# Performance work log

Measured on AMD Instinct MI355X. Metric: run time of the kernel, lower is better.

The kernel has to match this reference:

```python
import jax, jax.numpy as jnp
import numpy as np

HEADS = 8
D_K = 64
LN_EPS = 1e-6


def setup_inputs() -> dict:
    key = jax.random.key(0)
    ks = jax.random.split(key, 12)
    B, S, D = 4, 2048, 512
    inp = {
        "key": jax.random.normal(ks[0], (B, S, D), jnp.float32),
        "value": jax.random.normal(ks[1], (B, S, D), jnp.float32),
        "query": jax.random.normal(ks[2], (B, S, D), jnp.float32),
        "mask": jax.random.randint(ks[3], (B, S, S), 0, 2).astype(bool),
        # projection weights (torch Linear: y = x @ W.T + b)
        "Wk": jax.random.normal(ks[4], (D, D), jnp.float32) * (1.0 / np.sqrt(D)),
        "bk": jnp.zeros((D,), jnp.float32),
        "Wv": jax.random.normal(ks[5], (D, D), jnp.float32) * (1.0 / np.sqrt(D)),
        "bv": jnp.zeros((D,), jnp.float32),
        "Wq": jax.random.normal(ks[6], (D, D), jnp.float32) * (1.0 / np.sqrt(D)),
        "bq": jnp.zeros((D,), jnp.float32),
        # LayerNorm gain/bias
        "a2": jnp.ones((D,), jnp.float32),
        "b2": jnp.zeros((D,), jnp.float32),
    }
    return inp


def _attention(key, value, query, mask, Wk, bk, Wv, bv, Wq, bq, a2, b2):
    B, Sq, D = query.shape
    Sk = key.shape[1]
    H, dk = HEADS, D_K

    def split_heads(x, W, b):
        y = x @ W.T + b                                   # [B, S, D]
        return y.reshape(x.shape[0], x.shape[1], H, dk).transpose(0, 2, 1, 3)  # [B,H,S,dk]

    k_up = split_heads(key, Wk, bk)
    v_up = split_heads(value, Wv, bv)
    q_up = split_heads(query, Wq, bq)

    # scaled dot-product scores, full [B,H,Sq,Sk] matrix (as in the original bmm)
    scores = jnp.einsum("bhqd,bhkd->bhqk", q_up, k_up) / jnp.sqrt(jnp.asarray(dk, scores_dtype(q_up)))
    scores = jnp.where(mask[:, None, :, :], -jnp.inf, scores)
    attn = jax.nn.softmax(scores, axis=-1)                # dropout p=0 -> identity

    out = jnp.einsum("bhqk,bhkd->bhqd", attn, v_up)       # [B,H,Sq,dk]
    out = out.transpose(0, 2, 1, 3).reshape(B, Sq, D)
    res = out + query                                     # residual (res_dropout p=0)

    # OpenNMT LayerNorm: (x - mu) / (std + eps) * a2 + b2, unbiased std
    mu = res.mean(axis=-1, keepdims=True)
    var = jnp.sum((res - mu) ** 2, axis=-1, keepdims=True) / (D - 1)
    res = a2 * (res - mu) / (jnp.sqrt(var) + LN_EPS) + b2

    attn_flat = attn.reshape(B * H, Sq, Sk)               # matches torch [B*H, Sq, Sk]
    return res, attn_flat


def scores_dtype(x):
    return x.dtype


def reference(key, value, query, mask, Wk, bk, Wv, bv, Wq, bq, a2, b2):
    return _attention(key, value, query, mask, Wk, bk, Wv, bv, Wq, bq, a2, b2)
```

## Files before the change

### kernel.cpp

```cpp
#include <hip/hip_runtime.h>
#include <stdint.h>

typedef float f32x4 __attribute__((ext_vector_type(4)));
typedef short bf16x8 __attribute__((ext_vector_type(8)));

constexpr int NB = 4;
constexpr int NS = 2048;
constexpr int ND = 512;
constexpr int NH = 8;
constexpr int NDK = 64;
constexpr int NT = NS / 64;
constexpr float QSCALE = 0.125f * 1.44269504088896340736f;

static __device__ __forceinline__ unsigned short f2bf(float f) {
    union { float f; uint32_t u; } v; v.f = f;
    uint32_t r = (v.u + 0x7FFFu + ((v.u >> 16) & 1u)) >> 16;
    return (unsigned short)r;
}
static __device__ __forceinline__ uint32_t pkbf(float a, float b) {
    union { float f; uint32_t u; } x, y; x.f = a; y.f = b;
    return ((x.u + 0x8000u) >> 16) | (((y.u + 0x8000u) >> 16) << 16);
}
static __device__ __forceinline__ float exp2_fast(float x) {
#if __has_builtin(__builtin_amdgcn_exp2f)
    return __builtin_amdgcn_exp2f(x);
#else
    return exp2f(x);
#endif
}

static __device__ __forceinline__ void gload_lds16(const void* g, void* l) {
    __builtin_amdgcn_global_load_lds((const __attribute__((address_space(1))) void*)g,
                                     (__attribute__((address_space(3))) void*)l, 16, 0, 0);
}

__global__ __launch_bounds__(256) void cvt3_kernel(const float4* __restrict__ a,
                                                   const float4* __restrict__ b,
                                                   const float4* __restrict__ c,
                                                   ushort4* __restrict__ oa,
                                                   ushort4* __restrict__ ob,
                                                   ushort4* __restrict__ oc, int n4) {
    int which = blockIdx.y;
    const float4* in = which == 0 ? a : which == 1 ? b : c;
    ushort4* out = which == 0 ? oa : which == 1 ? ob : oc;
    int i = blockIdx.x * blockDim.x + threadIdx.x;
    if (i >= n4) return;
    float4 v = in[i];
    ushort4 o;
    o.x = f2bf(v.x); o.y = f2bf(v.y); o.z = f2bf(v.z); o.w = f2bf(v.w);
    out[i] = o;
}

__global__ __launch_bounds__(256) void bitmask_kernel(const int* __restrict__ mask,
                                                      unsigned long long* __restrict__ bm,
                                                      int nwords) {
    int lane = threadIdx.x & 63;
    int wave = threadIdx.x >> 6;
    int wgid = blockIdx.x * 4 + wave;
    int nw = gridDim.x * 4;
    for (int c = wgid; c < nwords; c += nw) {
        int v = mask[(size_t)c * 64 + lane];
        unsigned long long bits = __ballot(v != 0);
        if (lane == 0) bm[c] = bits;
    }
}

__global__ __launch_bounds__(256) void proj_kernel(const unsigned short* __restrict__ xq,
                                                   const unsigned short* __restrict__ xk,
                                                   const unsigned short* __restrict__ xv,
                                                   const unsigned short* __restrict__ wq,
                                                   const unsigned short* __restrict__ wk,
                                                   const unsigned short* __restrict__ wv,
                                                   const float* __restrict__ bq,
                                                   const float* __restrict__ bk,
                                                   const float* __restrict__ bv,
                                                   unsigned short* __restrict__ Qw,
                                                   unsigned short* __restrict__ Kw,
                                                   unsigned short* __restrict__ VTw) {
    int z = blockIdx.z;
    const unsigned short* X = z == 0 ? xq : z == 1 ? xk : xv;
    const unsigned short* W = z == 0 ? wq : z == 1 ? wk : wv;
    const float* bias = z == 0 ? bq : z == 1 ? bk : bv;
    unsigned short* out = z == 0 ? Qw : z == 1 ? Kw : VTw;
    float scale = z == 0 ? QSCALE : 1.0f;
    int vtrans = (z == 2);

    int lane = threadIdx.x & 63;
    int wave = threadIdx.x >> 6;
    int lrow = lane & 15, lgrp = lane >> 4;
    int m0 = blockIdx.x * 64 + wave * 16;
    int n0 = blockIdx.y * 64;

    f32x4 acc[4] = {{0.f,0.f,0.f,0.f},{0.f,0.f,0.f,0.f},{0.f,0.f,0.f,0.f},{0.f,0.f,0.f,0.f}};
    const unsigned short* xrow = X + (size_t)(m0 + lrow) * ND;
    for (int k = 0; k < ND; k += 32) {
        bf16x8 a = *(const bf16x8*)(xrow + k + lgrp * 8);
#pragma unroll
        for (int n = 0; n < 4; n++) {
            bf16x8 b = *(const bf16x8*)(W + (size_t)(n0 + n * 16 + lrow) * ND + k + lgrp * 8);
            acc[n] = __builtin_amdgcn_mfma_f32_16x16x32_bf16(a, b, acc[n], 0, 0, 0);
        }
    }
#pragma unroll
    for (int n = 0; n < 4; n++) {
        int col = n0 + n * 16 + lrow;
        int h = col >> 6, d = col & 63;
        float bv_ = bias[col];
#pragma unroll
        for (int j = 0; j < 4; j++) {
            int m = m0 + lgrp * 4 + j;
            int bidx = m >> 11, s = m & (NS - 1);
            float y = (acc[n][j] + bv_) * scale;
            size_t off = vtrans ? ((size_t)(bidx * NH + h) * NDK + d) * NS + s
                                : ((size_t)(bidx * NH + h) * NS + s) * NDK + d;
            out[off] = f2bf(y);
        }
    }
}

__global__ __launch_bounds__(512) void attn_kernel(const unsigned short* __restrict__ Q,
                                                   const unsigned short* __restrict__ K,
                                                   const unsigned short* __restrict__ VT,
                                                   const unsigned long long* __restrict__ bm,
                                                   float* __restrict__ attn_out,
                                                   float* __restrict__ Ob) {
    __shared__ __align__(16) unsigned short kb[2][64 * 64];
    __shared__ __align__(16) unsigned short vb[2][64 * 64];
    __shared__ __align__(16) unsigned short pl[8][16][72];

    int lane = threadIdx.x & 63;
    int wave = threadIdx.x >> 6;
    int lrow = lane & 15, lgrp = lane >> 4;

    int id = blockIdx.x;
    int xcd = id & 7;
    int loc = id >> 3;
    int bh = xcd * 4 + (loc >> 4);
    int qb = loc & 15;
    int b = bh >> 3, h = bh & 7;
    int qw = qb * 128 + wave * 16;

    const unsigned short* qrow = Q + ((size_t)bh * NS + qw + lrow) * NDK + lgrp * 8;
    bf16x8 aq0 = *(const bf16x8*)(qrow);
    bf16x8 aq1 = *(const bf16x8*)(qrow + 32);

    const unsigned short* kbase = K + (size_t)bh * NS * NDK;
    const unsigned short* vbase = VT + (size_t)bh * NDK * NS;
    const unsigned long long* bmrow = bm + ((size_t)b * NS + qw + lrow) * (NS / 64);

    int rl = lane >> 3, cc = lane & 7;
    int cs = (cc ^ rl) * 8;

    gload_lds16(kbase + (size_t)(8 * wave + rl) * NDK + cs, &kb[0][wave * 512]);
    unsigned long long wc = bmrow[0], wn = 0;
    asm volatile("s_waitcnt vmcnt(1)" ::: "memory");
    __builtin_amdgcn_s_barrier();

    float lacc = 0.f;
    for (int t = 0; t < NT; t++) {
        int buf = t & 1;
        if (t + 1 < NT) {
            gload_lds16(kbase + (size_t)((t + 1) * 64 + 8 * wave + rl) * NDK + cs,
                        &kb[buf ^ 1][wave * 512]);
            wn = bmrow[t + 1];
        }
        f32x4 sc[4] = {{0.f,0.f,0.f,0.f},{0.f,0.f,0.f,0.f},{0.f,0.f,0.f,0.f},{0.f,0.f,0.f,0.f}};
        __builtin_amdgcn_s_setprio(1);
#pragma unroll
        for (int n = 0; n < 4; n++) {
            int R = n * 16 + lrow;
            bf16x8 b0 = *(const bf16x8*)&kb[buf][R * 64 + ((lgrp ^ (lrow & 7)) * 8)];
            bf16x8 b1 = *(const bf16x8*)&kb[buf][R * 64 + (((4 + lgrp) ^ (lrow & 7)) * 8)];
            sc[n] = __builtin_amdgcn_mfma_f32_16x16x32_bf16(b0, aq0, sc[n], 0, 0, 0);
            sc[n] = __builtin_amdgcn_mfma_f32_16x16x32_bf16(b1, aq1, sc[n], 0, 0, 0);
        }
        __builtin_amdgcn_s_setprio(0);
        uint32_t wlo = (uint32_t)wc, whi = (uint32_t)(wc >> 32);
#pragma unroll
        for (int n = 0; n < 4; n++)
#pragma unroll
            for (int j = 0; j < 4; j++) {
                uint32_t bit = ((n < 2 ? wlo : whi) >> ((n & 1) * 16 + lgrp * 4 + j)) & 1u;
                float e = exp2_fast(sc[n][j]);
                lacc += bit ? 0.f : e;
            }
        wc = wn;
        if (t + 1 < NT) {
            asm volatile("s_waitcnt vmcnt(1)" ::: "memory");
            __builtin_amdgcn_s_barrier();
        }
    }
    lacc += __shfl_xor(lacc, 16);
    lacc += __shfl_xor(lacc, 32);
    float li = -__log2f(lacc);

    gload_lds16(kbase + (size_t)(8 * wave + rl) * NDK + cs, &kb[0][wave * 512]);
    gload_lds16(vbase + (size_t)(8 * wave + rl) * NS + cs, &vb[0][wave * 512]);
    wc = bmrow[0];
    asm volatile("s_waitcnt vmcnt(1)" ::: "memory");
    __builtin_amdgcn_s_barrier();

    f32x4 accO[4] = {{0.f,0.f,0.f,0.f},{0.f,0.f,0.f,0.f},{0.f,0.f,0.f,0.f},{0.f,0.f,0.f,0.f}};
    float* arow = attn_out + (size_t)bh * NS * NS + (size_t)(qw + lrow) * NS;

    for (int t = 0; t < NT; t++) {
        int buf = t & 1;
        int kt = t * 64;
        if (t + 1 < NT) {
            gload_lds16(kbase + (size_t)((t + 1) * 64 + 8 * wave + rl) * NDK + cs,
                        &kb[buf ^ 1][wave * 512]);
            gload_lds16(vbase + (size_t)(8 * wave + rl) * NS + (t + 1) * 64 + cs,
                        &vb[buf ^ 1][wave * 512]);
            wn = bmrow[t + 1];
        }
        f32x4 sc[4] = {{0.f,0.f,0.f,0.f},{0.f,0.f,0.f,0.f},{0.f,0.f,0.f,0.f},{0.f,0.f,0.f,0.f}};
        __builtin_amdgcn_s_setprio(1);
#pragma unroll
        for (int n = 0; n < 4; n++) {
            int R = n * 16 + lrow;
            bf16x8 b0 = *(const bf16x8*)&kb[buf][R * 64 + ((lgrp ^ (lrow & 7)) * 8)];
            bf16x8 b1 = *(const bf16x8*)&kb[buf][R * 64 + (((4 + lgrp) ^ (lrow & 7)) * 8)];
            sc[n] = __builtin_amdgcn_mfma_f32_16x16x32_bf16(b0, aq0, sc[n], 0, 0, 0);
            sc[n] = __builtin_amdgcn_mfma_f32_16x16x32_bf16(b1, aq1, sc[n], 0, 0, 0);
        }
        __builtin_amdgcn_s_setprio(0);
        uint32_t wlo = (uint32_t)wc, whi = (uint32_t)(wc >> 32);
#pragma unroll
        for (int n = 0; n < 4; n++) {
            float p0, p1, p2, p3;
            uint32_t wsel = (n < 2) ? wlo : whi;
            int base = (n & 1) * 16 + lgrp * 4;
            p0 = ((wsel >> (base + 0)) & 1u) ? 0.f : exp2_fast(sc[n][0] + li);
            p1 = ((wsel >> (base + 1)) & 1u) ? 0.f : exp2_fast(sc[n][1] + li);
            p2 = ((wsel >> (base + 2)) & 1u) ? 0.f : exp2_fast(sc[n][2] + li);
            p3 = ((wsel >> (base + 3)) & 1u) ? 0.f : exp2_fast(sc[n][3] + li);
            f32x4 pv4 = {p0, p1, p2, p3};
            __builtin_nontemporal_store(pv4, (f32x4*)(arow + kt + n * 16 + lgrp * 4));
            uint2 pk = {pkbf(p0, p1), pkbf(p2, p3)};
            *(uint2*)&pl[wave][lrow][n * 16 + lgrp * 4] = pk;
        }
        __builtin_amdgcn_s_setprio(1);
#pragma unroll
        for (int step = 0; step < 2; step++) {
            bf16x8 ap = *(const bf16x8*)&pl[wave][lrow][step * 32 + lgrp * 8];
#pragma unroll
            for (int n = 0; n < 4; n++) {
                int R = n * 16 + lrow;
                bf16x8 bv = *(const bf16x8*)&vb[buf][R * 64 + (((4 * step + lgrp) ^ (lrow & 7)) * 8)];
                accO[n] = __builtin_amdgcn_mfma_f32_16x16x32_bf16(ap, bv, accO[n], 0, 0, 0);
            }
        }
        __builtin_amdgcn_s_setprio(0);
        wc = wn;
        if (t + 1 < NT) {
            asm volatile("s_waitcnt vmcnt(5)" ::: "memory");
            __builtin_amdgcn_s_barrier();
        }
    }

#pragma unroll
    for (int n = 0; n < 4; n++)
#pragma unroll
        for (int j = 0; j < 4; j++) {
            int qi = qw + lgrp * 4 + j;
            Ob[((size_t)b * NS + qi) * ND + h * NDK + n * 16 + lrow] = accO[n][j];
        }
}

__global__ __launch_bounds__(256) void ln_kernel(const float* __restrict__ Ob,
                                                 const float* __restrict__ query,
                                                 const float* __restrict__ a2,
                                                 const float* __restrict__ b2,
                                                 float* __restrict__ out) {
    int row = blockIdx.x * 4 + (threadIdx.x >> 6);
    int lane = threadIdx.x & 63;
    const float4* orow = (const float4*)(Ob + (size_t)row * ND);
    const float4* qrow = (const float4*)(query + (size_t)row * ND);
    float4 v[2];
    float sum = 0.f;
#pragma unroll
    for (int t = 0; t < 2; t++) {
        float4 o = orow[lane + t * 64];
        float4 q = qrow[lane + t * 64];
        v[t].x = o.x + q.x; v[t].y = o.y + q.y; v[t].z = o.z + q.z; v[t].w = o.w + q.w;
        sum += v[t].x + v[t].y + v[t].z + v[t].w;
    }
#pragma unroll
    for (int s = 1; s < 64; s <<= 1) sum += __shfl_xor(sum, s);
    float mu = sum * (1.f / ND);
    float sq = 0.f;
#pragma unroll
    for (int t = 0; t < 2; t++) {
        float dx = v[t].x - mu, dy = v[t].y - mu, dz = v[t].z - mu, dw = v[t].w - mu;
        sq += dx * dx + dy * dy + dz * dz + dw * dw;
    }
#pragma unroll
    for (int s = 1; s < 64; s <<= 1) sq += __shfl_xor(sq, s);
    float var = sq * (1.f / (ND - 1));
    float inv = 1.f / (sqrtf(var) + 1e-6f);
    float4* orow_out = (float4*)(out + (size_t)row * ND);
#pragma unroll
    for (int t = 0; t < 2; t++) {
        float4 g = ((const float4*)a2)[lane + t * 64];
        float4 bb = ((const float4*)b2)[lane + t * 64];
        float4 r;
        r.x = g.x * (v[t].x - mu) * inv + bb.x;
        r.y = g.y * (v[t].y - mu) * inv + bb.y;
        r.z = g.z * (v[t].z - mu) * inv + bb.z;
        r.w = g.w * (v[t].w - mu) * inv + bb.w;
        orow_out[lane + t * 64] = r;
    }
}

extern "C" void kernel_launch(void* const* d_in, const int* in_sizes, int n_in,
                              void* d_out, int out_size, void* d_ws, size_t ws_size,
                              hipStream_t stream) {
    const float* key   = (const float*)d_in[0];
    const float* value = (const float*)d_in[1];
    const float* query = (const float*)d_in[2];
    const int*   mask  = (const int*)d_in[3];
    const float* Wk = (const float*)d_in[4];
    const float* bk = (const float*)d_in[5];
    const float* Wv = (const float*)d_in[6];
    const float* bv = (const float*)d_in[7];
    const float* Wq = (const float*)d_in[8];
    const float* bq = (const float*)d_in[9];
    const float* a2 = (const float*)d_in[10];
    const float* b2 = (const float*)d_in[11];

    const size_t nX = (size_t)NB * NS * ND;
    const size_t nW = (size_t)ND * ND;
    const int    nBMw = NB * NS * NS / 64;

    unsigned short* xq  = (unsigned short*)d_ws;
    unsigned short* xk  = xq + nX;
    unsigned short* xv  = xk + nX;
    unsigned short* wqb = xv + nX;
    unsigned short* wkb = wqb + nW;
    unsigned short* wvb = wkb + nW;
    unsigned short* Qw  = wvb + nW;
    unsigned short* Kw  = Qw + nX;
    unsigned short* VTw = Kw + nX;
    float* Ow = (float*)(VTw + nX);
    unsigned long long* bmw = (unsigned long long*)(Ow + nX);

    bitmask_kernel<<<2048, 256, 0, stream>>>(mask, bmw, nBMw);

    cvt3_kernel<<<dim3((int)(nX / 4 / 256), 3), 256, 0, stream>>>(
        (const float4*)query, (const float4*)key, (const float4*)value,
        (ushort4*)xq, (ushort4*)xk, (ushort4*)xv, (int)(nX / 4));
    cvt3_kernel<<<dim3((int)(nW / 4 / 256), 3), 256, 0, stream>>>(
        (const float4*)Wq, (const float4*)Wk, (const float4*)Wv,
        (ushort4*)wqb, (ushort4*)wkb, (ushort4*)wvb, (int)(nW / 4));

    proj_kernel<<<dim3(128, 8, 3), 256, 0, stream>>>(xq, xk, xv, wqb, wkb, wvb,
                                                     bq, bk, bv, Qw, Kw, VTw);

    float* attn_out = (float*)d_out + nX;
    attn_kernel<<<512, 512, 0, stream>>>(Qw, Kw, VTw, bmw, attn_out, Ow);

    ln_kernel<<<2048, 256, 0, stream>>>(Ow, query, a2, b2, (float*)d_out);
}
```

Measured before the change: 362.7 us.

## Split softmax row-sum pass into separate key-split kernel with atomic accumulation

The first pass of the attention kernel, which computes each query row's exp-sum over all keys, moves into its own kernel. That kernel splits the key range four ways across a second grid dimension and adds partial sums into a zeroed buffer with atomics. The attention kernel then reads the finished row sums and runs only the second pass. The goal is more parallelism for the serial row-sum pass, since the main kernel launches only 512 blocks. In exchange there is an extra memset and launch, K is read directly from global memory without LDS staging, and atomics make the float summation order nondeterministic.

```diff
diff --git a/kernel.cpp b/kernel.cpp
--- a/kernel.cpp
+++ b/kernel.cpp
@@ -118,10 +118,61 @@
     }
 }
 
+__global__ __launch_bounds__(512) void lsum_kernel(const unsigned short* __restrict__ Q,
+                                                   const unsigned short* __restrict__ K,
+                                                   const unsigned long long* __restrict__ bm,
+                                                   float* __restrict__ lsum) {
+    int lane = threadIdx.x & 63;
+    int wave = threadIdx.x >> 6;
+    int lrow = lane & 15, lgrp = lane >> 4;
+
+    int id = blockIdx.x;
+    int xcd = id & 7;
+    int loc = id >> 3;
+    int bh = xcd * 4 + (loc >> 4);
+    int qb = loc & 15;
+    int b = bh >> 3;
+    int qw = qb * 128 + wave * 16;
+    int kt0 = blockIdx.y * (NS / 4), kt1 = kt0 + NS / 4;
+
+    const unsigned short* qrow = Q + ((size_t)bh * NS + qw + lrow) * NDK + lgrp * 8;
+    bf16x8 aq0 = *(const bf16x8*)(qrow);
+    bf16x8 aq1 = *(const bf16x8*)(qrow + 32);
+    const unsigned short* kbase = K + (size_t)bh * NS * NDK;
+    const unsigned long long* bmrow = bm + ((size_t)b * NS + qw + lrow) * (NS / 64);
+
+    float lacc = 0.f;
+    for (int kt = kt0; kt < kt1; kt += 64) {
+        unsigned long long w = bmrow[kt >> 6];
+        f32x4 sc[4] = {{0.f,0.f,0.f,0.f},{0.f,0.f,0.f,0.f},{0.f,0.f,0.f,0.f},{0.f,0.f,0.f,0.f}};
+#pragma unroll
+        for (int n = 0; n < 4; n++) {
+            const unsigned short* kr = kbase + (size_t)(kt + n * 16 + lrow) * NDK + lgrp * 8;
+            bf16x8 b0 = *(const bf16x8*)kr;
+            bf16x8 b1 = *(const bf16x8*)(kr + 32);
+            sc[n] = __builtin_amdgcn_mfma_f32_16x16x32_bf16(b0, aq0, sc[n], 0, 0, 0);
+            sc[n] = __builtin_amdgcn_mfma_f32_16x16x32_bf16(b1, aq1, sc[n], 0, 0, 0);
+        }
+        uint32_t wlo = (uint32_t)w, whi = (uint32_t)(w >> 32);
+#pragma unroll
+        for (int n = 0; n < 4; n++)
+#pragma unroll
+            for (int j = 0; j < 4; j++) {
+                uint32_t bit = ((n < 2 ? wlo : whi) >> ((n & 1) * 16 + lgrp * 4 + j)) & 1u;
+                float e = exp2_fast(sc[n][j]);
+                lacc += bit ? 0.f : e;
+            }
+    }
+    lacc += __shfl_xor(lacc, 16);
+    lacc += __shfl_xor(lacc, 32);
+    if (lane < 16) atomicAdd(&lsum[(size_t)bh * NS + qw + lane], lacc);
+}
+
 __global__ __launch_bounds__(512) void attn_kernel(const unsigned short* __restrict__ Q,
                                                    const unsigned short* __restrict__ K,
                                                    const unsigned short* __restrict__ VT,
                                                    const unsigned long long* __restrict__ bm,
+                                                   const float* __restrict__ lsum,
                                                    float* __restrict__ attn_out,
                                                    float* __restrict__ Ob) {
     __shared__ __align__(16) unsigned short kb[2][64 * 64];
@@ -140,6 +191,9 @@
     int b = bh >> 3, h = bh & 7;
     int qw = qb * 128 + wave * 16;
 
+    float lrow_l = lsum[(size_t)bh * NS + qw + lrow];
+    float li = -__log2f(lrow_l);
+
     const unsigned short* qrow = Q + ((size_t)bh * NS + qw + lrow) * NDK + lgrp * 8;
     bf16x8 aq0 = *(const bf16x8*)(qrow);
     bf16x8 aq1 = *(const bf16x8*)(qrow + 32);
@@ -152,51 +206,8 @@
     int cs = (cc ^ rl) * 8;
 
     gload_lds16(kbase + (size_t)(8 * wave + rl) * NDK + cs, &kb[0][wave * 512]);
+    gload_lds16(vbase + (size_t)(8 * wave + rl) * NS + cs, &vb[0][wave * 512]);
     unsigned long long wc = bmrow[0], wn = 0;
-    asm volatile("s_waitcnt vmcnt(1)" ::: "memory");
-    __builtin_amdgcn_s_barrier();
-
-    float lacc = 0.f;
-    for (int t = 0; t < NT; t++) {
-        int buf = t & 1;
-        if (t + 1 < NT) {
-            gload_lds16(kbase + (size_t)((t + 1) * 64 + 8 * wave + rl) * NDK + cs,
-                        &kb[buf ^ 1][wave * 512]);
-            wn = bmrow[t + 1];
-        }
-        f32x4 sc[4] = {{0.f,0.f,0.f,0.f},{0.f,0.f,0.f,0.f},{0.f,0.f,0.f,0.f},{0.f,0.f,0.f,0.f}};
-        __builtin_amdgcn_s_setprio(1);
-#pragma unroll
-        for (int n = 0; n < 4; n++) {
-            int R = n * 16 + lrow;
-            bf16x8 b0 = *(const bf16x8*)&kb[buf][R * 64 + ((lgrp ^ (lrow & 7)) * 8)];
-            bf16x8 b1 = *(const bf16x8*)&kb[buf][R * 64 + (((4 + lgrp) ^ (lrow & 7)) * 8)];
-            sc[n] = __builtin_amdgcn_mfma_f32_16x16x32_bf16(b0, aq0, sc[n], 0, 0, 0);
-            sc[n] = __builtin_amdgcn_mfma_f32_16x16x32_bf16(b1, aq1, sc[n], 0, 0, 0);
-        }
-        __builtin_amdgcn_s_setprio(0);
-        uint32_t wlo = (uint32_t)wc, whi = (uint32_t)(wc >> 32);
-#pragma unroll
-        for (int n = 0; n < 4; n++)
-#pragma unroll
-            for (int j = 0; j < 4; j++) {
-                uint32_t bit = ((n < 2 ? wlo : whi) >> ((n & 1) * 16 + lgrp * 4 + j)) & 1u;
-                float e = exp2_fast(sc[n][j]);
-                lacc += bit ? 0.f : e;
-            }
-        wc = wn;
-        if (t + 1 < NT) {
-            asm volatile("s_waitcnt vmcnt(1)" ::: "memory");
-            __builtin_amdgcn_s_barrier();
-        }
-    }
-    lacc += __shfl_xor(lacc, 16);
-    lacc += __shfl_xor(lacc, 32);
-    float li = -__log2f(lacc);
-
-    gload_lds16(kbase + (size_t)(8 * wave + rl) * NDK + cs, &kb[0][wave * 512]);
-    gload_lds16(vbase + (size_t)(8 * wave + rl) * NS + cs, &vb[0][wave * 512]);
-    wc = bmrow[0];
     asm volatile("s_waitcnt vmcnt(1)" ::: "memory");
     __builtin_amdgcn_s_barrier();
 
@@ -343,6 +354,9 @@
     unsigned short* VTw = Kw + nX;
     float* Ow = (float*)(VTw + nX);
     unsigned long long* bmw = (unsigned long long*)(Ow + nX);
+    float* lbuf = (float*)(bmw + nBMw);
+
+    hipMemsetAsync(lbuf, 0, (size_t)NB * NH * NS * sizeof(float), stream);
 
     bitmask_kernel<<<2048, 256, 0, stream>>>(mask, bmw, nBMw);
 
@@ -356,8 +370,10 @@
     proj_kernel<<<dim3(128, 8, 3), 256, 0, stream>>>(xq, xk, xv, wqb, wkb, wvb,
                                                      bq, bk, bv, Qw, Kw, VTw);
 
+    lsum_kernel<<<dim3(512, 4), 512, 0, stream>>>(Qw, Kw, bmw, lbuf);
+
     float* attn_out = (float*)d_out + nX;
-    attn_kernel<<<512, 512, 0, stream>>>(Qw, Kw, VTw, bmw, attn_out, Ow);
+    attn_kernel<<<512, 512, 0, stream>>>(Qw, Kw, VTw, bmw, lbuf, attn_out, Ow);
 
     ln_kernel<<<2048, 256, 0, stream>>>(Ow, query, a2, b2, (float*)d_out);
 }
```

New measurement: 469.7 us. 1.29x slower.
